# Kernel optimization log

Measured on AMD Instinct MI355X. Metric: run time of the kernel, lower is better.

The kernel has to match this reference:

```python
import jax, jax.numpy as jnp
import numpy as np

B, S, D, E, H, K = 64, 2048, 1024, 32, 4096, 8


def setup_inputs() -> dict:
    key = jax.random.key(0)
    k0, k1, k2, k3 = jax.random.split(key, 4)
    x = jax.random.normal(k0, (B, S, D), jnp.float32)
    # gate: nn.Linear(D, E) -> weight [E, D], bias [E]
    gate_w = jax.random.normal(k1, (E, D), jnp.float32) * (1.0 / np.sqrt(D))
    gate_b = jnp.zeros((E,), jnp.float32)
    # expert weights include the bias row (input dim + 1)
    w1 = jax.random.normal(k2, (E, D + 1, H), jnp.float32) * (1.0 / np.sqrt(D + 1))
    w2 = jax.random.normal(k3, (E, H + 1, D), jnp.float32) * (1.0 / np.sqrt(H + 1))
    return {"x": x, "gate_w": gate_w, "gate_b": gate_b, "w1": w1, "w2": w2}


def reference(x, gate_w, gate_b, w1, w2):
    b, s, d = x.shape
    # gating: softmax over the TOKEN axis (expert-choice routing)
    logits = jnp.einsum('bsd,ed->bse', x, gate_w) + gate_b          # [b, s, E]
    probs = jax.nn.softmax(logits, axis=-2)                          # softmax over tokens
    # top-k tokens per expert (torch.topk over dim=-2)
    vals_t, idx_t = jax.lax.top_k(probs.transpose(0, 2, 1), K)      # [b, E, k]
    vals = vals_t.transpose(0, 2, 1)                                 # [b, k, E]
    idx = idx_t.transpose(0, 2, 1)                                   # [b, k, E]
    flat_idx = idx.reshape(b, K * E)                                 # gather order: [k, E] flattened
    # gather selected tokens
    tok = jnp.take_along_axis(x, flat_idx[:, :, None], axis=1)       # [b, k*E, d]
    tok = tok.reshape(b, K, E, d)
    # weighted merge (mux) of the k tokens per expert
    merged = jnp.einsum('bked,bke->bed', tok, vals)                  # [b, E, d]
    ones = jnp.ones(merged.shape[:-1] + (1,), merged.dtype)
    # expert FFN (bias folded into the extra weight row)
    h = jnp.einsum('bei,eih->beh', jnp.concatenate([merged, ones], -1), w1)
    h = jax.nn.gelu(h, approximate=False)                            # torch nn.GELU() = exact erf
    o = jnp.einsum('bej,ejo->beo', jnp.concatenate([h, ones], -1), w2)  # [b, E, d]
    # demux: broadcast expert output back to its k tokens, weighted, scatter-add
    out_tok = jnp.einsum('beo,bke->bkeo', o, vals).reshape(b, K * E, d)
    out = jnp.zeros_like(x).at[jnp.arange(b)[:, None], flat_idx].add(out_tok)
    return out
```

## Files before the change

kernel.cpp:

```cpp
#include <hip/hip_runtime.h>
#include <hip/hip_bf16.h>
#include <math.h>

constexpr int NB = 64;
constexpr int NS = 2048;
constexpr int ND = 1024;
constexpr int NE = 32;
constexpr int NH = 4096;
constexpr int NK = 8;

typedef short bf16x8 __attribute__((ext_vector_type(8)));
typedef float f32x4  __attribute__((ext_vector_type(4)));

__device__ __forceinline__ unsigned short f2bf_rne(float v) {
  unsigned u = __builtin_bit_cast(unsigned, v);
  u += 0x7fffu + ((u >> 16) & 1u);
  return (unsigned short)(u >> 16);
}
__device__ __forceinline__ void split2(float v, unsigned short& h, unsigned short& l) {
  unsigned u = __builtin_bit_cast(unsigned, v);
  h = (unsigned short)(u >> 16);
  float fh = __builtin_bit_cast(float, u & 0xffff0000u);
  l = f2bf_rne(v - fh);
}

__device__ __forceinline__ void gload_lds16(const void* g, void* l) {
  __builtin_amdgcn_global_load_lds(
      (const __attribute__((address_space(1))) unsigned*)g,
      (__attribute__((address_space(3))) unsigned*)l, 16, 0, 0);
}

__global__ __launch_bounds__(256) void k_gate_mfma(const float* __restrict__ x,
                                                   const float* __restrict__ gw,
                                                   float* __restrict__ logitsT) {
  const int b  = blockIdx.y;
  const int s0 = blockIdx.x * 128;
  const int t  = threadIdx.x;
  const int l  = t & 63;
  const int w  = t >> 6;

  __shared__ char smem[40960];
  short* Ah = (short*)smem;
  short* Al = (short*)(smem + 16384);
  short* Bh = (short*)(smem + 32768);
  short* Bl = (short*)(smem + 36864);
  float* trans = (float*)smem;

  f32x4 acc[2][2] = {};

  const int xr_ = t >> 4, xc = (t & 15) * 4;
  const int ge = t >> 3,  gk = (t & 7) * 8;

  float xreg[8][4];
  float wreg[8];

  auto issue = [&](int k0) {
#pragma unroll
    for (int p = 0; p < 8; ++p) {
      const int r = p * 16 + xr_;
      *(float4*)xreg[p] = *(const float4*)&x[((size_t)b * NS + s0 + r) * ND + k0 + xc];
    }
    *(float4*)&wreg[0] = *(const float4*)&gw[(size_t)ge * ND + k0 + gk];
    *(float4*)&wreg[4] = *(const float4*)&gw[(size_t)ge * ND + k0 + gk + 4];
  };
  auto commit = [&]() {
#pragma unroll
    for (int p = 0; p < 8; ++p) {
      const int r = p * 16 + xr_;
      unsigned short h[4], lo[4];
#pragma unroll
      for (int j = 0; j < 4; ++j) split2(xreg[p][j], h[j], lo[j]);
      const int off = r * 64 + (xc ^ ((r & 7) * 8));
      *(ushort4*)&Ah[off] = make_ushort4(h[0], h[1], h[2], h[3]);
      *(ushort4*)&Al[off] = make_ushort4(lo[0], lo[1], lo[2], lo[3]);
    }
    unsigned short h8[8], l8[8];
#pragma unroll
    for (int j = 0; j < 8; ++j) split2(wreg[j], h8[j], l8[j]);
    const int boff = ge * 64 + (gk ^ ((ge & 7) * 8));
    *(uint4*)&Bh[boff] = *(const uint4*)h8;
    *(uint4*)&Bl[boff] = *(const uint4*)l8;
  };

  issue(0);
  for (int k0 = 0; k0 < ND; k0 += 64) {
    commit();
    __syncthreads();
    if (k0 + 64 < ND) issue(k0 + 64);
#pragma unroll
    for (int ks = 0; ks < 2; ++ks) {
      const int koff = ks * 32 + (l >> 4) * 8;
      bf16x8 ah[2], alo[2], bh[2], blo[2];
#pragma unroll
      for (int mf = 0; mf < 2; ++mf) {
        const int r   = w * 32 + mf * 16 + (l & 15);
        const int off = r * 64 + (koff ^ ((r & 7) * 8));
        ah[mf]  = *(const bf16x8*)&Ah[off];
        alo[mf] = *(const bf16x8*)&Al[off];
      }
#pragma unroll
      for (int nf = 0; nf < 2; ++nf) {
        const int n   = nf * 16 + (l & 15);
        const int off = n * 64 + (koff ^ ((n & 7) * 8));
        bh[nf]  = *(const bf16x8*)&Bh[off];
        blo[nf] = *(const bf16x8*)&Bl[off];
      }
#pragma unroll
      for (int mf = 0; mf < 2; ++mf)
#pragma unroll
        for (int nf = 0; nf < 2; ++nf) {
          acc[mf][nf] = __builtin_amdgcn_mfma_f32_16x16x32_bf16(ah[mf],  bh[nf],  acc[mf][nf], 0, 0, 0);
          acc[mf][nf] = __builtin_amdgcn_mfma_f32_16x16x32_bf16(alo[mf], bh[nf],  acc[mf][nf], 0, 0, 0);
          acc[mf][nf] = __builtin_amdgcn_mfma_f32_16x16x32_bf16(ah[mf],  blo[nf], acc[mf][nf], 0, 0, 0);
        }
    }
    __syncthreads();
  }
#pragma unroll
  for (int mf = 0; mf < 2; ++mf)
#pragma unroll
    for (int nf = 0; nf < 2; ++nf)
#pragma unroll
      for (int j = 0; j < 4; ++j) {
        const int sl = w * 32 + mf * 16 + (l >> 4) * 4 + j;
        const int ec = nf * 16 + (l & 15);
        trans[sl * 33 + ec] = acc[mf][nf][j];
      }
  __syncthreads();
  const int eo = t >> 3, sc = (t & 7) * 16;
#pragma unroll
  for (int j4 = 0; j4 < 4; ++j4) {
    float4 v;
    v.x = trans[(sc + j4 * 4 + 0) * 33 + eo];
    v.y = trans[(sc + j4 * 4 + 1) * 33 + eo];
    v.z = trans[(sc + j4 * 4 + 2) * 33 + eo];
    v.w = trans[(sc + j4 * 4 + 3) * 33 + eo];
    *(float4*)&logitsT[((size_t)b * NE + eo) * NS + s0 + sc + j4 * 4] = v;
  }
}

__global__ __launch_bounds__(256) void k_topk(const float* __restrict__ logitsT,
                                              const float* __restrict__ x,
                                              const float* __restrict__ gw,
                                              float* __restrict__ tval,
                                              int* __restrict__ tidx) {
  const int be = blockIdx.x, b = be >> 5, e = be & 31;
  const float* row = logitsT + (size_t)be * NS;
  const int t = threadIdx.x, w = t >> 6, lane = t & 63;

  __shared__ float  cv[64];
  __shared__ int    cix[64];
  __shared__ double wsum[4];
  __shared__ float  smax;
  __shared__ int    gci[16];
  __shared__ float  glc[16];
  __shared__ double ginv;

  float v[8]; int si[8];
#pragma unroll
  for (int j = 0; j < 8; ++j) {
    const int s = w * 512 + lane + j * 64;
    v[j] = row[s]; si[j] = s;
  }
#pragma unroll
  for (int i = 0; i < 7; ++i)
#pragma unroll
    for (int j = 0; j < 7 - i; ++j) {
      const bool sw = (v[j + 1] > v[j]) || (v[j + 1] == v[j] && si[j + 1] < si[j]);
      const float tv = sw ? v[j + 1] : v[j];
      const int   ti = sw ? si[j + 1] : si[j];
      v[j + 1] = sw ? v[j] : v[j + 1];  si[j + 1] = sw ? si[j] : si[j + 1];
      v[j] = tv;  si[j] = ti;
    }
  const float mxl = v[0];
  double s8 = 1.0;
#pragma unroll
  for (int j = 1; j < 8; ++j) s8 += (double)expf(v[j] - mxl);

  for (int r = 0; r < 16; ++r) {
    float bp = v[0]; int bi = si[0]; int bl = lane;
#pragma unroll
    for (int off = 1; off < 64; off <<= 1) {
      const float op = __shfl_xor(bp, off);
      const int   oi = __shfl_xor(bi, off);
      const int   ol = __shfl_xor(bl, off);
      if (op > bp || (op == bp && oi < bi)) { bp = op; bi = oi; bl = ol; }
    }
    if (lane == 0) { cv[w * 16 + r] = bp; cix[w * 16 + r] = bi; }
    if (lane == bl) {
      v[0]=v[1]; v[1]=v[2]; v[2]=v[3]; v[3]=v[4]; v[4]=v[5]; v[5]=v[6]; v[6]=v[7]; v[7]=-INFINITY;
      si[0]=si[1]; si[1]=si[2]; si[2]=si[3]; si[3]=si[4]; si[4]=si[5]; si[5]=si[6]; si[6]=si[7]; si[7]=0x7fffffff;
    }
  }
  __syncthreads();
  if (w == 0) {
    float mv = cv[lane]; int mi = cix[lane];
    for (int r = 0; r < 16; ++r) {
      float bp = mv; int bi = mi; int bl = lane;
#pragma unroll
      for (int off = 1; off < 64; off <<= 1) {
        const float op = __shfl_xor(bp, off);
        const int   oi = __shfl_xor(bi, off);
        const int   ol = __shfl_xor(bl, off);
        if (op > bp || (op == bp && oi < bi)) { bp = op; bi = oi; bl = ol; }
      }
      if (lane == 0) { gci[r] = bi; if (r == 0) smax = bp; }
      if (lane == bl) { mv = -INFINITY; mi = 0x7fffffff; }
    }
  }
  __syncthreads();
  const float mx = smax;
  double lsum = s8 * (double)expf(mxl - mx);
#pragma unroll
  for (int off = 32; off; off >>= 1) lsum += __shfl_xor(lsum, off);
  if (lane == 0) wsum[w] = lsum;
  __syncthreads();
  if (t == 0) ginv = 1.0 / (wsum[0] + wsum[1] + wsum[2] + wsum[3]);

  const int kb = lane * 16;
  float gwl[16];
  *(float4*)&gwl[0]  = *(const float4*)&gw[(size_t)e * ND + kb];
  *(float4*)&gwl[4]  = *(const float4*)&gw[(size_t)e * ND + kb + 4];
  *(float4*)&gwl[8]  = *(const float4*)&gw[(size_t)e * ND + kb + 8];
  *(float4*)&gwl[12] = *(const float4*)&gw[(size_t)e * ND + kb + 12];
#pragma unroll
  for (int q = 0; q < 4; ++q) {
    const int c = w * 4 + q;
    const int ciq = gci[c];
    const float* xr = x + ((size_t)b * NS + ciq) * ND + kb;
    float xv[16];
    *(float4*)&xv[0]  = *(const float4*)&xr[0];
    *(float4*)&xv[4]  = *(const float4*)&xr[4];
    *(float4*)&xv[8]  = *(const float4*)&xr[8];
    *(float4*)&xv[12] = *(const float4*)&xr[12];
    double d = 0.0;
#pragma unroll
    for (int j2 = 0; j2 < 16; ++j2) d += (double)xv[j2] * (double)gwl[j2];
#pragma unroll
    for (int off = 32; off; off >>= 1) d += __shfl_xor(d, off);
    if (lane == 0) glc[c] = (float)d;
  }
  __syncthreads();
  if (t < 16) {
    const float mylc = glc[t]; const int myci = gci[t];
    int rank = 0;
#pragma unroll
    for (int c2 = 0; c2 < 16; ++c2) {
      if (c2 == t) continue;
      rank += (glc[c2] > mylc) || (glc[c2] == mylc && gci[c2] < myci);
    }
    if (rank < 8) {
      tval[be * 8 + rank] = (float)((double)expf(mylc - mx) * ginv);
      tidx[be * 8 + rank] = myci;
    }
  }
}

__global__ __launch_bounds__(256) void k_merge(const float* __restrict__ x,
                                               const float* __restrict__ tval,
                                               const int* __restrict__ tidx,
                                               unsigned short* __restrict__ A1) {
  const int be = blockIdx.x;
  const int b  = be >> 5;
  const int e  = be & 31;
  const int t  = threadIdx.x;
  float4 acc = {0.f, 0.f, 0.f, 0.f};
#pragma unroll
  for (int k = 0; k < 8; ++k) {
    float v = tval[be * 8 + k];
    int   s = tidx[be * 8 + k];
    float4 xv = *(const float4*)&x[((size_t)b * NS + s) * ND + t * 4];
    acc.x += v * xv.x; acc.y += v * xv.y; acc.z += v * xv.z; acc.w += v * xv.w;
  }
  const int kt = t >> 4;
  const int g  = (t & 15) >> 1;
  const size_t off = ((size_t)(e * 16 + kt)) * 4096 + b * 64 + ((g ^ (b & 7)) << 3) + (t & 1) * 4;
  unsigned short h4[4] = {f2bf_rne(acc.x), f2bf_rne(acc.y), f2bf_rne(acc.z), f2bf_rne(acc.w)};
  *(ushort4*)&A1[off] = *(const ushort4*)h4;
}

template <int K, int N, bool GELU>
__global__ __launch_bounds__(256, 4) void k_ffn(const unsigned short* __restrict__ AT,
                                                const float* __restrict__ W,
                                                unsigned short* __restrict__ OT,
                                                float* __restrict__ Of) {
  constexpr int KT = K / 64;
  const int e  = blockIdx.y;
  const int n0 = blockIdx.x * 64;
  const int t  = threadIdx.x, l = t & 63, w = t >> 6;
  const int wr = w >> 1, wc = w & 1;

  __shared__ char smem[32768];

  const float* Wbase = W + (size_t)e * (K + 1) * N;
  f32x4 acc[2][2] = {};

  const int wn  = l;
  const int wk0 = w * 8;
  float wreg[2][8];

  auto issueW = [&](int kt) {
    const float* Wg = Wbase + (size_t)(kt * 64) * N + n0 + wn;
#pragma unroll
    for (int rn = 0; rn < 2; ++rn)
#pragma unroll
      for (int j = 0; j < 8; ++j)
        wreg[rn][j] = Wg[(size_t)(wk0 + rn * 32 + j) * N];
  };
  auto issueA = [&](int kt, int dst) {
    const unsigned short* at = AT + ((size_t)(e * KT + kt)) * 4096;
    char* Ab = smem + dst * 8192;
#pragma unroll
    for (int p = 0; p < 2; ++p)
      gload_lds16(at + p * 2048 + t * 8, Ab + p * 4096 + w * 1024);
  };
  auto commitW = [&](int dst) {
    short* Bb = (short*)(smem + 16384 + dst * 8192);
#pragma unroll
    for (int rn = 0; rn < 2; ++rn) {
      const int kr = (wk0 + rn * 32) >> 3;
      unsigned short s8[8];
#pragma unroll
      for (int j = 0; j < 8; ++j) s8[j] = f2bf_rne(wreg[rn][j]);
      *(uint4*)&Bb[wn * 64 + ((kr ^ (wn & 7)) << 3)] = *(const uint4*)s8;
    }
  };
  auto mfma_phase = [&](int cur) {
    const short* Ab = (const short*)(smem + cur * 8192);
    const short* Bb = (const short*)(smem + 16384 + cur * 8192);
#pragma unroll
    for (int ks = 0; ks < 2; ++ks) {
      const int g8 = ks * 4 + (l >> 4);
      bf16x8 a[2], bb[2];
#pragma unroll
      for (int mf = 0; mf < 2; ++mf) {
        const int m = wr * 32 + mf * 16 + (l & 15);
        a[mf] = *(const bf16x8*)&Ab[m * 64 + ((g8 ^ (m & 7)) << 3)];
      }
#pragma unroll
      for (int nf = 0; nf < 2; ++nf) {
        const int n = wc * 32 + nf * 16 + (l & 15);
        bb[nf] = *(const bf16x8*)&Bb[n * 64 + ((g8 ^ (n & 7)) << 3)];
      }
#pragma unroll
      for (int mf = 0; mf < 2; ++mf)
#pragma unroll
        for (int nf = 0; nf < 2; ++nf)
          acc[mf][nf] = __builtin_amdgcn_mfma_f32_16x16x32_bf16(a[mf], bb[nf], acc[mf][nf], 0, 0, 0);
    }
  };

  issueW(0); issueA(0, 0);
  commitW(0);
  __syncthreads();
  if (KT > 1) { issueW(1); issueA(1, 1); }
  int cur = 0;
  for (int kt = 0; kt < KT; ++kt) {
    mfma_phase(cur);
    if (kt + 1 < KT) {
      commitW(cur ^ 1);
      __syncthreads();
      if (kt + 2 < KT) { issueW(kt + 2); issueA(kt + 2, cur); }
      cur ^= 1;
    }
  }
  __syncthreads();

  if (GELU) {
    unsigned short* transU = (unsigned short*)smem;
#pragma unroll
    for (int nf = 0; nf < 2; ++nf) {
      const int c = wc * 32 + nf * 16 + (l & 15);
      const float bias = Wbase[(size_t)K * N + n0 + c];
#pragma unroll
      for (int mf = 0; mf < 2; ++mf)
#pragma unroll
        for (int j = 0; j < 4; ++j) {
          const int m = wr * 32 + mf * 16 + (l >> 4) * 4 + j;
          float vv = acc[mf][nf][j] + bias;
          vv = 0.5f * vv * (1.0f + erff(vv * 0.70710678118654752440f));
          transU[m * 72 + c] = f2bf_rne(vv);
        }
    }
    __syncthreads();
    const int m  = t >> 2;
    const int c0 = (t & 3) * 16;
    const size_t tb = ((size_t)(e * (N / 64) + blockIdx.x)) * 4096;
    uint4 v0 = *(const uint4*)&transU[m * 72 + c0];
    uint4 v1 = *(const uint4*)&transU[m * 72 + c0 + 8];
    const int g0 = c0 >> 3;
    *(uint4*)&OT[tb + m * 64 + ((g0 ^ (m & 7)) << 3)]       = v0;
    *(uint4*)&OT[tb + m * 64 + (((g0 + 1) ^ (m & 7)) << 3)] = v1;
  } else {
    float* transF = (float*)smem;
#pragma unroll
    for (int nf = 0; nf < 2; ++nf) {
      const int c = wc * 32 + nf * 16 + (l & 15);
      const float bias = Wbase[(size_t)K * N + n0 + c];
#pragma unroll
      for (int mf = 0; mf < 2; ++mf)
#pragma unroll
        for (int j = 0; j < 4; ++j) {
          const int m = wr * 32 + mf * 16 + (l >> 4) * 4 + j;
          transF[m * 68 + c] = acc[mf][nf][j] + bias;
        }
    }
    __syncthreads();
    const int m  = t >> 2;
    const int c0 = (t & 3) * 16;
    float* og = Of + ((size_t)m * NE + e) * ND + n0 + c0;
    *(float4*)&og[0]  = *(const float4*)&transF[m * 68 + c0];
    *(float4*)&og[4]  = *(const float4*)&transF[m * 68 + c0 + 4];
    *(float4*)&og[8]  = *(const float4*)&transF[m * 68 + c0 + 8];
    *(float4*)&og[12] = *(const float4*)&transF[m * 68 + c0 + 12];
  }
}

__global__ __launch_bounds__(256) void k_scatter(const float* __restrict__ Obuf,
                                                 const float* __restrict__ tval,
                                                 const int* __restrict__ tidx,
                                                 float* __restrict__ out) {
  const int s = blockIdx.x;
  const int b = blockIdx.y;
  const int t = threadIdx.x;
  __shared__ unsigned long long masks[4];

  const int myIdx = tidx[b * 256 + t];
  unsigned long long m = __ballot(myIdx == s);
  if ((t & 63) == 0) masks[t >> 6] = m;
  __syncthreads();

  float4 acc = {0.f, 0.f, 0.f, 0.f};
#pragma unroll
  for (int w = 0; w < 4; ++w) {
    unsigned long long mm = masks[w];
    while (mm) {
      int bit = __ffsll(mm) - 1;
      mm &= mm - 1;
      int r = w * 64 + bit;
      float v = tval[b * 256 + r];
      const float4 ov = *(const float4*)&Obuf[((size_t)b * NE + (r >> 3)) * ND + t * 4];
      acc.x += v * ov.x; acc.y += v * ov.y; acc.z += v * ov.z; acc.w += v * ov.w;
    }
  }
  *(float4*)&out[((size_t)b * NS + s) * ND + t * 4] = acc;
}

extern "C" void kernel_launch(void* const* d_in, const int* in_sizes, int n_in,
                              void* d_out, int out_size, void* d_ws, size_t ws_size,
                              hipStream_t stream) {
  const float* x  = (const float*)d_in[0];
  const float* gw = (const float*)d_in[1];
  const float* w1 = (const float*)d_in[3];
  const float* w2 = (const float*)d_in[4];
  float* out = (float*)d_out;

  char* ws = (char*)d_ws;
  float* logitsT     = (float*)ws;
  float* tval        = (float*)(ws + 16777216);
  int*   tidx        = (int*)  (ws + 16842752);
  unsigned short* A1 = (unsigned short*)(ws + 16908288);
  unsigned short* Hb = (unsigned short*)(ws + 21102592);
  float* Obuf        = (float*)(ws + 37879808);

  k_gate_mfma<<<dim3(NS / 128, NB), 256, 0, stream>>>(x, gw, logitsT);
  k_topk<<<NB * NE, 256, 0, stream>>>(logitsT, x, gw, tval, tidx);
  k_merge<<<NB * NE, 256, 0, stream>>>(x, tval, tidx, A1);
  k_ffn<ND, NH, true ><<<dim3(NH / 64, NE), 256, 0, stream>>>(A1, w1, Hb, nullptr);
  k_ffn<NH, ND, false><<<dim3(ND / 64, NE), 256, 0, stream>>>(Hb, w2, nullptr, Obuf);
  k_scatter<<<dim3(NS, NB), 256, 0, stream>>>(Obuf, tval, tidx, out);
}
```

Baseline: 587.9 us.

## Use single-bf16 gate GEMM with double buffering, pipeline FFN loads, batch scatter rows

The gate GEMM drops the split hi/lo bf16 emulation of fp32 and uses a single bf16 MFMA per product instead of three. Its shared-memory tiles become double-buffered so the next tile's global loads overlap the current MFMAs. The FFN k-loop is restructured to issue the next tile's loads before computing the current one. The scatter kernel now handles 8 sequence positions per block instead of one, cutting block count and reloads of tidx. Lowering gate logits to plain bf16 risks changing top-k token selection when probabilities are close.

```diff
diff --git a/kernel.cpp b/kernel.cpp
--- a/kernel.cpp
+++ b/kernel.cpp
@@ -16,12 +16,6 @@
   unsigned u = __builtin_bit_cast(unsigned, v);
   u += 0x7fffu + ((u >> 16) & 1u);
   return (unsigned short)(u >> 16);
-}
-__device__ __forceinline__ void split2(float v, unsigned short& h, unsigned short& l) {
-  unsigned u = __builtin_bit_cast(unsigned, v);
-  h = (unsigned short)(u >> 16);
-  float fh = __builtin_bit_cast(float, u & 0xffff0000u);
-  l = f2bf_rne(v - fh);
 }
 
 __device__ __forceinline__ void gload_lds16(const void* g, void* l) {
@@ -40,10 +34,6 @@
   const int w  = t >> 6;
 
   __shared__ char smem[40960];
-  short* Ah = (short*)smem;
-  short* Al = (short*)(smem + 16384);
-  short* Bh = (short*)(smem + 32768);
-  short* Bl = (short*)(smem + 36864);
   float* trans = (float*)smem;
 
   f32x4 acc[2][2] = {};
@@ -54,7 +44,8 @@
   float xreg[8][4];
   float wreg[8];
 
-  auto issue = [&](int k0) {
+  auto issue = [&](int kt) {
+    const int k0 = kt * 64;
 #pragma unroll
     for (int p = 0; p < 8; ++p) {
       const int r = p * 16 + xr_;
@@ -63,59 +54,62 @@
     *(float4*)&wreg[0] = *(const float4*)&gw[(size_t)ge * ND + k0 + gk];
     *(float4*)&wreg[4] = *(const float4*)&gw[(size_t)ge * ND + k0 + gk + 4];
   };
-  auto commit = [&]() {
+  auto commit = [&](int dst) {
+    short* Ah = (short*)(smem + dst * 16384);
+    short* Bh = (short*)(smem + 32768 + dst * 4096);
 #pragma unroll
     for (int p = 0; p < 8; ++p) {
       const int r = p * 16 + xr_;
-      unsigned short h[4], lo[4];
-#pragma unroll
-      for (int j = 0; j < 4; ++j) split2(xreg[p][j], h[j], lo[j]);
+      unsigned short h[4];
+#pragma unroll
+      for (int j = 0; j < 4; ++j) h[j] = f2bf_rne(xreg[p][j]);
       const int off = r * 64 + (xc ^ ((r & 7) * 8));
-      *(ushort4*)&Ah[off] = make_ushort4(h[0], h[1], h[2], h[3]);
-      *(ushort4*)&Al[off] = make_ushort4(lo[0], lo[1], lo[2], lo[3]);
-    }
-    unsigned short h8[8], l8[8];
-#pragma unroll
-    for (int j = 0; j < 8; ++j) split2(wreg[j], h8[j], l8[j]);
+      *(ushort4*)&Ah[off] = *(const ushort4*)h;
+    }
+    unsigned short h8[8];
+#pragma unroll
+    for (int j = 0; j < 8; ++j) h8[j] = f2bf_rne(wreg[j]);
     const int boff = ge * 64 + (gk ^ ((ge & 7) * 8));
     *(uint4*)&Bh[boff] = *(const uint4*)h8;
-    *(uint4*)&Bl[boff] = *(const uint4*)l8;
-  };
-
-  issue(0);
-  for (int k0 = 0; k0 < ND; k0 += 64) {
-    commit();
-    __syncthreads();
-    if (k0 + 64 < ND) issue(k0 + 64);
+  };
+  auto mfma_phase = [&](int cur) {
+    const short* Ah = (const short*)(smem + cur * 16384);
+    const short* Bh = (const short*)(smem + 32768 + cur * 4096);
 #pragma unroll
     for (int ks = 0; ks < 2; ++ks) {
       const int koff = ks * 32 + (l >> 4) * 8;
-      bf16x8 ah[2], alo[2], bh[2], blo[2];
+      bf16x8 a[2], bb[2];
 #pragma unroll
       for (int mf = 0; mf < 2; ++mf) {
-        const int r   = w * 32 + mf * 16 + (l & 15);
-        const int off = r * 64 + (koff ^ ((r & 7) * 8));
-        ah[mf]  = *(const bf16x8*)&Ah[off];
-        alo[mf] = *(const bf16x8*)&Al[off];
+        const int r = w * 32 + mf * 16 + (l & 15);
+        a[mf] = *(const bf16x8*)&Ah[r * 64 + (koff ^ ((r & 7) * 8))];
       }
 #pragma unroll
       for (int nf = 0; nf < 2; ++nf) {
-        const int n   = nf * 16 + (l & 15);
-        const int off = n * 64 + (koff ^ ((n & 7) * 8));
-        bh[nf]  = *(const bf16x8*)&Bh[off];
-        blo[nf] = *(const bf16x8*)&Bl[off];
+        const int n = nf * 16 + (l & 15);
+        bb[nf] = *(const bf16x8*)&Bh[n * 64 + (koff ^ ((n & 7) * 8))];
       }
 #pragma unroll
       for (int mf = 0; mf < 2; ++mf)
 #pragma unroll
-        for (int nf = 0; nf < 2; ++nf) {
-          acc[mf][nf] = __builtin_amdgcn_mfma_f32_16x16x32_bf16(ah[mf],  bh[nf],  acc[mf][nf], 0, 0, 0);
-          acc[mf][nf] = __builtin_amdgcn_mfma_f32_16x16x32_bf16(alo[mf], bh[nf],  acc[mf][nf], 0, 0, 0);
-          acc[mf][nf] = __builtin_amdgcn_mfma_f32_16x16x32_bf16(ah[mf],  blo[nf], acc[mf][nf], 0, 0, 0);
-        }
-    }
+        for (int nf = 0; nf < 2; ++nf)
+          acc[mf][nf] = __builtin_amdgcn_mfma_f32_16x16x32_bf16(a[mf], bb[nf], acc[mf][nf], 0, 0, 0);
+    }
+  };
+
+  issue(0);
+  commit(0);
+  __syncthreads();
+  int cur = 0;
+  for (int kt = 0; kt < ND / 64; ++kt) {
+    const bool more = (kt + 1 < ND / 64);
+    if (more) issue(kt + 1);
+    mfma_phase(cur);
+    if (more) commit(cur ^ 1);
     __syncthreads();
-  }
+    cur ^= 1;
+  }
+
 #pragma unroll
   for (int mf = 0; mf < 2; ++mf)
 #pragma unroll
@@ -353,18 +347,15 @@
   issueW(0); issueA(0, 0);
   commitW(0);
   __syncthreads();
-  if (KT > 1) { issueW(1); issueA(1, 1); }
   int cur = 0;
   for (int kt = 0; kt < KT; ++kt) {
+    const bool more = (kt + 1 < KT);
+    if (more) { issueW(kt + 1); issueA(kt + 1, cur ^ 1); }
     mfma_phase(cur);
-    if (kt + 1 < KT) {
-      commitW(cur ^ 1);
-      __syncthreads();
-      if (kt + 2 < KT) { issueW(kt + 2); issueA(kt + 2, cur); }
-      cur ^= 1;
-    }
-  }
-  __syncthreads();
+    if (more) commitW(cur ^ 1);
+    __syncthreads();
+    cur ^= 1;
+  }
 
   if (GELU) {
     unsigned short* transU = (unsigned short*)smem;
@@ -420,30 +411,37 @@
                                                  const float* __restrict__ tval,
                                                  const int* __restrict__ tidx,
                                                  float* __restrict__ out) {
-  const int s = blockIdx.x;
-  const int b = blockIdx.y;
-  const int t = threadIdx.x;
-  __shared__ unsigned long long masks[4];
+  const int s0 = blockIdx.x * 8;
+  const int b  = blockIdx.y;
+  const int t  = threadIdx.x;
+  const int w  = t >> 6;
+  __shared__ unsigned long long masks[8][4];
 
   const int myIdx = tidx[b * 256 + t];
-  unsigned long long m = __ballot(myIdx == s);
-  if ((t & 63) == 0) masks[t >> 6] = m;
-  __syncthreads();
-
-  float4 acc = {0.f, 0.f, 0.f, 0.f};
-#pragma unroll
-  for (int w = 0; w < 4; ++w) {
-    unsigned long long mm = masks[w];
-    while (mm) {
-      int bit = __ffsll(mm) - 1;
-      mm &= mm - 1;
-      int r = w * 64 + bit;
-      float v = tval[b * 256 + r];
-      const float4 ov = *(const float4*)&Obuf[((size_t)b * NE + (r >> 3)) * ND + t * 4];
-      acc.x += v * ov.x; acc.y += v * ov.y; acc.z += v * ov.z; acc.w += v * ov.w;
-    }
-  }
-  *(float4*)&out[((size_t)b * NS + s) * ND + t * 4] = acc;
+#pragma unroll
+  for (int j = 0; j < 8; ++j) {
+    unsigned long long m = __ballot(myIdx == s0 + j);
+    if ((t & 63) == 0) masks[j][w] = m;
+  }
+  __syncthreads();
+
+#pragma unroll
+  for (int j = 0; j < 8; ++j) {
+    float4 acc = {0.f, 0.f, 0.f, 0.f};
+#pragma unroll
+    for (int q = 0; q < 4; ++q) {
+      unsigned long long mm = masks[j][q];
+      while (mm) {
+        int bit = __ffsll(mm) - 1;
+        mm &= mm - 1;
+        int r = q * 64 + bit;
+        float v = tval[b * 256 + r];
+        const float4 ov = *(const float4*)&Obuf[((size_t)b * NE + (r >> 3)) * ND + t * 4];
+        acc.x += v * ov.x; acc.y += v * ov.y; acc.z += v * ov.z; acc.w += v * ov.w;
+      }
+    }
+    *(float4*)&out[((size_t)b * NS + s0 + j) * ND + t * 4] = acc;
+  }
 }
 
 extern "C" void kernel_launch(void* const* d_in, const int* in_sizes, int n_in,
@@ -468,5 +466,5 @@
   k_merge<<<NB * NE, 256, 0, stream>>>(x, tval, tidx, A1);
   k_ffn<ND, NH, true ><<<dim3(NH / 64, NE), 256, 0, stream>>>(A1, w1, Hb, nullptr);
   k_ffn<NH, ND, false><<<dim3(ND / 64, NE), 256, 0, stream>>>(Hb, w2, nullptr, Obuf);
-  k_scatter<<<dim3(NS, NB), 256, 0, stream>>>(Obuf, tval, tidx, out);
-}
+  k_scatter<<<dim3(NS / 8, NB), 256, 0, stream>>>(Obuf, tval, tidx, out);
+}
```

Result: faster. 570.9 us (-2.9%).
